# Optimization experiments

Hardware: AMD Instinct MI355X
Metric: run time of the kernel (lower is better)

## Reference

```python
import jax, jax.numpy as jnp
import numpy as np

N = 100000      # nodes
E = 1250000     # edges
F_IN = 32       # node_feat_dim
H = 64          # hidden_dim (hard-coded in module)
R = 8           # num_relations
G = 256         # graphs in batch
EMB = 16        # embedding_dim
OUT = 1         # output_dim
EPS = 1e-5


def setup_inputs() -> dict:
    key = jax.random.key(0)
    ks = jax.random.split(key, 40)
    w = lambda k, shape: (jax.random.normal(k, shape, jnp.float32) * 0.05)
    inp = {
        'x': jax.random.normal(ks[0], (N, F_IN), jnp.float32),
        'edge_index': jax.random.randint(ks[1], (2, E), 0, N),
        'edge_type': jax.random.randint(ks[2], (E,), 0, R),
        'batch': jnp.sort(jax.random.randint(ks[3], (N,), 0, G)),
        # RGCN layer params: per-relation weight, root weight, bias
        'conv1_w': w(ks[4], (R, F_IN, H)), 'conv1_root': w(ks[5], (F_IN, H)), 'conv1_b': jnp.zeros((H,), jnp.float32),
        'bn1_g': jnp.ones((H,), jnp.float32), 'bn1_b': jnp.zeros((H,), jnp.float32),
        'conv2_w': w(ks[6], (R, H, H)), 'conv2_root': w(ks[7], (H, H)), 'conv2_b': jnp.zeros((H,), jnp.float32),
        'bn2_g': jnp.ones((H,), jnp.float32), 'bn2_b': jnp.zeros((H,), jnp.float32),
        'conv3_w': w(ks[8], (R, H, H)), 'conv3_root': w(ks[9], (H, H)), 'conv3_b': jnp.zeros((H,), jnp.float32),
        'bn3_g': jnp.ones((H,), jnp.float32), 'bn3_b': jnp.zeros((H,), jnp.float32),
        # fc_emb: Linear(384->128), BN(128), LeakyReLU, Dropout(eval=id), Linear(128->EMB)
        'fc1_w': w(ks[10], (3 * H * 2, 128)), 'fc1_b': jnp.zeros((128,), jnp.float32),
        'fcbn_g': jnp.ones((128,), jnp.float32), 'fcbn_b': jnp.zeros((128,), jnp.float32),
        'fc2_w': w(ks[11], (128, EMB)), 'fc2_b': jnp.zeros((EMB,), jnp.float32),
        # decoder: Linear(EMB->64), LeakyReLU, Linear(64->OUT)
        'dec1_w': w(ks[12], (EMB, 64)), 'dec1_b': jnp.zeros((64,), jnp.float32),
        'dec2_w': w(ks[13], (64, OUT)), 'dec2_b': jnp.zeros((OUT,), jnp.float32),
    }
    return inp


def _leaky(z):
    return jnp.where(z > 0, z, 0.2 * z)


def _bn(x, g, b):  # training-mode batch norm, biased variance
    mu = x.mean(axis=0)
    var = x.var(axis=0)
    return g * (x - mu) * jax.lax.rsqrt(var + EPS) + b


def _rgcn(x, W, root, bias, src, dst, edge_type):
    # out_i = x_i @ root + bias + sum_r mean_{j in N_r(i)} x_j @ W_r
    out = x @ root + bias
    for r in range(R):
        mask = (edge_type == r).astype(x.dtype)           # [E]
        h = x @ W[r]                                      # [N, out]
        msg = h[src] * mask[:, None]                      # gather + mask
        s = jax.ops.segment_sum(msg, dst, num_segments=N)  # scatter-add
        cnt = jax.ops.segment_sum(mask, dst, num_segments=N)
        out = out + s / jnp.maximum(cnt, 1.0)[:, None]
    return out


def reference(x, edge_index, edge_type, batch,
              conv1_w, conv1_root, conv1_b, bn1_g, bn1_b,
              conv2_w, conv2_root, conv2_b, bn2_g, bn2_b,
              conv3_w, conv3_root, conv3_b, bn3_g, bn3_b,
              fc1_w, fc1_b, fcbn_g, fcbn_b, fc2_w, fc2_b,
              dec1_w, dec1_b, dec2_w, dec2_b):
    src, dst = edge_index[0], edge_index[1]
    x1 = jax.nn.relu(_bn(_rgcn(x, conv1_w, conv1_root, conv1_b, src, dst, edge_type), bn1_g, bn1_b))
    x2 = jax.nn.relu(_bn(_rgcn(x1, conv2_w, conv2_root, conv2_b, src, dst, edge_type), bn2_g, bn2_b))
    x3 = jax.nn.relu(_bn(_rgcn(x2, conv3_w, conv3_root, conv3_b, src, dst, edge_type), bn3_g, bn3_b))
    x_all = jnp.concatenate([x1, x2, x3], axis=1)         # [N, 3H]
    ones = jnp.ones((N,), x.dtype)
    cnt = jax.ops.segment_sum(ones, batch, num_segments=G)
    pool_mean = jax.ops.segment_sum(x_all, batch, num_segments=G) / jnp.maximum(cnt, 1.0)[:, None]
    pool_max = jax.ops.segment_max(x_all, batch, num_segments=G)
    pool_max = jnp.where(jnp.isfinite(pool_max), pool_max, 0.0)
    x_graph = jnp.concatenate([pool_mean, pool_max], axis=1)  # [G, 6H]
    h = _leaky(_bn(x_graph @ fc1_w + fc1_b, fcbn_g, fcbn_b))  # dropout = identity (eval)
    emb = h @ fc2_w + fc2_b                                   # [G, EMB]
    pred = _leaky(emb @ dec1_w + dec1_b) @ dec2_w + dec2_b    # [G, OUT]
    return (pred, emb)
```

## Files before the change

kernel.cpp:

```cpp
#include <hip/hip_runtime.h>

#define NN 100000
#define NE 1250000
#define FIN 32
#define HD 64
#define NR 8
#define NG 256
#define BN_EPS 1e-5f
#define PCH 100
#define M_KEYS (NN * NR)
#define NB 782
#define RREP 32
#define HW 576

#if defined(__has_builtin)
#if __has_builtin(__builtin_amdgcn_fdot2_f32_bf16)
#define USE_DOT2 1
#endif
#endif
#ifndef USE_DOT2
#define USE_DOT2 0
#endif

typedef unsigned short ushort_t;
typedef __attribute__((ext_vector_type(8))) short short8;
typedef __attribute__((ext_vector_type(4))) float f32x4;
typedef __attribute__((ext_vector_type(4))) unsigned int u32x4;
#if USE_DOT2
typedef __bf16 bf16x2 __attribute__((ext_vector_type(2)));
#endif

static __device__ __forceinline__ ushort_t f2bf(float f) {
  unsigned u = __float_as_uint(f);
  u += 0x7fffu + ((u >> 16) & 1u);
  return (ushort_t)(u >> 16);
}
static __device__ __forceinline__ float bf2f(ushort_t b) {
  return __uint_as_float((unsigned)b << 16);
}

__global__ void k_zero(float* __restrict__ p, int n) {
  int i = blockIdx.x * 256 + threadIdx.x;
  if (i < n) p[i] = 0.0f;
}

__global__ void k_cnt(const int* __restrict__ dst, const int* __restrict__ ty,
                      unsigned* __restrict__ cnt, int* __restrict__ rank) {
  int e = blockIdx.x * 256 + threadIdx.x;
  if (e < NE) {
    int key = dst[e] * NR + ty[e];
    rank[e] = (int)atomicAdd(&cnt[key], 1u);
  }
}

__global__ void k_scanA(const unsigned* __restrict__ cnt, unsigned* __restrict__ bsum) {
  __shared__ unsigned red[256];
  int t = threadIdx.x;
  int base = blockIdx.x * 1024 + t * 4;
  unsigned s = 0;
  #pragma unroll
  for (int i = 0; i < 4; i++) {
    int idx = base + i;
    if (idx < M_KEYS) s += cnt[idx];
  }
  red[t] = s;
  __syncthreads();
  for (int off = 128; off > 0; off >>= 1) {
    if (t < off) red[t] += red[t + off];
    __syncthreads();
  }
  if (t == 0) bsum[blockIdx.x] = red[0];
}

__global__ __launch_bounds__(1024) void k_scanB(const unsigned* __restrict__ bsum,
                                                unsigned* __restrict__ boff,
                                                int* __restrict__ rowstart) {
  __shared__ unsigned sb[1024];
  int t = threadIdx.x;
  unsigned mine = (t < NB) ? bsum[t] : 0u;
  sb[t] = mine;
  __syncthreads();
  for (int off = 1; off < 1024; off <<= 1) {
    unsigned v = (t >= off) ? sb[t - off] : 0u;
    __syncthreads();
    sb[t] += v;
    __syncthreads();
  }
  if (t < NB) boff[t] = sb[t] - mine;
  if (t == 1023) rowstart[M_KEYS] = (int)sb[1023];
}

__global__ void k_scanC(const unsigned* __restrict__ cnt, const unsigned* __restrict__ boff,
                        int* __restrict__ rowstart) {
  __shared__ unsigned sb[256];
  int t = threadIdx.x;
  int base = blockIdx.x * 1024 + t * 4;
  unsigned c0 = (base + 0 < M_KEYS) ? cnt[base + 0] : 0u;
  unsigned c1 = (base + 1 < M_KEYS) ? cnt[base + 1] : 0u;
  unsigned c2 = (base + 2 < M_KEYS) ? cnt[base + 2] : 0u;
  unsigned c3 = (base + 3 < M_KEYS) ? cnt[base + 3] : 0u;
  unsigned tot = c0 + c1 + c2 + c3;
  sb[t] = tot;
  __syncthreads();
  for (int off = 1; off < 256; off <<= 1) {
    unsigned v = (t >= off) ? sb[t - off] : 0u;
    __syncthreads();
    sb[t] += v;
    __syncthreads();
  }
  unsigned run = boff[blockIdx.x] + (sb[t] - tot);
  if (base + 0 < M_KEYS) rowstart[base + 0] = (int)run; run += c0;
  if (base + 1 < M_KEYS) rowstart[base + 1] = (int)run; run += c1;
  if (base + 2 < M_KEYS) rowstart[base + 2] = (int)run; run += c2;
  if (base + 3 < M_KEYS) rowstart[base + 3] = (int)run;
}

__global__ void k_place(const int* __restrict__ src, const int* __restrict__ dst,
                        const int* __restrict__ ty, const int* __restrict__ rank,
                        const int* __restrict__ rowstart, unsigned* __restrict__ eb) {
  int e = blockIdx.x * 256 + threadIdx.x;
  if (e < NE) {
    int t = ty[e];
    int key = dst[e] * NR + t;
    unsigned off = (unsigned)(src[e] * HW + t * 64);
    eb[rowstart[key] + rank[e]] = (off << 3) | (unsigned)t;
  }
}

template <int F>
__global__ void k_wconv(const float* __restrict__ convw, const float* __restrict__ root,
                        ushort_t* __restrict__ wt) {
  int i = blockIdx.x * 256 + threadIdx.x;
  if (i >= 576 * F) return;
  int c = i / F, k = i % F;
  float v = (c < 512) ? convw[((size_t)(c >> 6) * F + k) * 64 + (c & 63)]
                      : root[(size_t)k * 64 + (c & 63)];
  wt[(size_t)c * F + k] = f2bf(v);
}

template <int F, bool APPLY_BN>
__global__ __launch_bounds__(256) void k_xmm(
    const float* __restrict__ xin, const float* __restrict__ scsh,
    const ushort_t* __restrict__ wt, ushort_t* __restrict__ h) {
  constexpr int KK = 2 * F;
  constexpr int XPAD = KK + 8;
  constexpr int LDR = 592;
  __shared__ ushort_t xs[16 * XPAD];
  __shared__ ushort_t ot[16 * LDR];
  int lane = threadIdx.x & 63;
  int w = threadIdx.x >> 6;
  int m = lane & 15;
  int q = lane >> 4;
  int ct0 = w * 9;

  short8 bfrag[9 * (F / 32)];
  #pragma unroll
  for (int ks = 0; ks < F / 32; ks++)
    #pragma unroll
    for (int t = 0; t < 9; t++)
      bfrag[ks * 9 + t] =
          *(const short8*)(wt + (size_t)((ct0 + t) * 16 + m) * F + ks * 32 + q * 8);

  for (int tile = blockIdx.x; tile < NN / 16; tile += gridDim.x) {
    int nbase = tile * 16;
    for (int i = threadIdx.x; i < 16 * F; i += 256) {
      int r = i / F, k = i - r * F;
      float v = xin[(size_t)(nbase + r) * F + k];
      if (APPLY_BN) v = fmaxf(fmaf(v, scsh[k], scsh[64 + k]), 0.0f);
      ushort_t hi = f2bf(v);
      xs[r * XPAD + k] = hi;
      xs[r * XPAD + F + k] = f2bf(v - bf2f(hi));
    }
    __syncthreads();

    short8 afrag[2 * (F / 32)];
    #pragma unroll
    for (int ks = 0; ks < F / 32; ks++) {
      afrag[2 * ks + 0] = *(const short8*)&xs[m * XPAD + ks * 32 + q * 8];
      afrag[2 * ks + 1] = *(const short8*)&xs[m * XPAD + F + ks * 32 + q * 8];
    }

    f32x4 acc[9];
    #pragma unroll
    for (int t = 0; t < 9; t++) acc[t] = (f32x4){0.f, 0.f, 0.f, 0.f};
    #pragma unroll
    for (int ks = 0; ks < F / 32; ks++) {
      #pragma unroll
      for (int t = 0; t < 9; t++) {
        acc[t] = __builtin_amdgcn_mfma_f32_16x16x32_bf16(afrag[2 * ks + 0],
                                                         bfrag[ks * 9 + t], acc[t], 0, 0, 0);
        acc[t] = __builtin_amdgcn_mfma_f32_16x16x32_bf16(afrag[2 * ks + 1],
                                                         bfrag[ks * 9 + t], acc[t], 0, 0, 0);
      }
    }
    #pragma unroll
    for (int t = 0; t < 9; t++) {
      int col = (ct0 + t) * 16 + m;
      #pragma unroll
      for (int j = 0; j < 4; j++) {
        int row = q * 4 + j;
        ot[row * LDR + col] = f2bf(acc[t][j]);
      }
    }
    __syncthreads();
    u32x4* dst = (u32x4*)(h + (size_t)nbase * HW);
    for (int idx = threadIdx.x; idx < 16 * 72; idx += 256) {
      int row = idx / 72, i = idx - row * 72;
      dst[row * 72 + i] = *(const u32x4*)&ot[row * LDR + i * 8];
    }
  }
}

__global__ __launch_bounds__(256) void k_agg4(
    const ushort_t* __restrict__ h, const int* __restrict__ rs,
    const unsigned* __restrict__ eb, const float* __restrict__ bias,
    float* __restrict__ outp, float* __restrict__ statsrep) {
  __shared__ float red[1024];
  __shared__ ushort_t iclu[8][8];
  int lane = threadIdx.x & 63, w = threadIdx.x >> 6;
  int hw = lane >> 5;
  int nd = w * 2 + hw;
  int n = blockIdx.x * 8 + nd;
  int l32 = lane & 31;
  if (l32 < 8) {
    int c = rs[n * NR + l32 + 1] - rs[n * NR + l32];
    iclu[nd][l32] = f2bf(1.0f / (float)(c > 1 ? c : 1));
  }
  int lo = rs[n * NR];
  int cnt = rs[n * NR + NR] - lo;
  __syncthreads();
  int g = (lane >> 3) & 3;
  int c8 = (lane & 7) * 8;
  int cntmax = max(cnt, __shfl_xor(cnt, 32));
  float a[8];
  #pragma unroll
  for (int j = 0; j < 8; j++) a[j] = 0.f;
  for (int base = 0; base < cntmax; base += 16) {
    unsigned rec[4]; u32x4 hv[4]; unsigned icb[4];
    #pragma unroll
    for (int s = 0; s < 4; s++) {
      int el = base + s * 4 + g;
      int ee = (el < cnt) ? el : (cnt > 0 ? cnt - 1 : 0);
      rec[s] = eb[lo + ee];
      icb[s] = (el < cnt) ? (unsigned)iclu[nd][rec[s] & 7] : 0u;
    }
    #pragma unroll
    for (int s = 0; s < 4; s++)
      hv[s] = *(const u32x4*)(h + (size_t)(rec[s] >> 3) + c8);
#if USE_DOT2
    #pragma unroll
    for (int s = 0; s < 4; s += 2) {
      unsigned b01 = __builtin_amdgcn_perm(icb[s + 1], icb[s], 0x05040100u);
      bf16x2 bb = __builtin_bit_cast(bf16x2, b01);
      #pragma unroll
      for (int k = 0; k < 4; k++) {
        unsigned plo = __builtin_amdgcn_perm(hv[s + 1][k], hv[s][k], 0x05040100u);
        unsigned phi = __builtin_amdgcn_perm(hv[s + 1][k], hv[s][k], 0x07060302u);
        a[2 * k + 0] = __builtin_amdgcn_fdot2_f32_bf16(
            __builtin_bit_cast(bf16x2, plo), bb, a[2 * k + 0], false);
        a[2 * k + 1] = __builtin_amdgcn_fdot2_f32_bf16(
            __builtin_bit_cast(bf16x2, phi), bb, a[2 * k + 1], false);
      }
    }
#else
    #pragma unroll
    for (int s = 0; s < 4; s++) {
      float ic = bf2f((ushort_t)icb[s]);
      #pragma unroll
      for (int k = 0; k < 4; k++) {
        a[2 * k + 0] = fmaf(__uint_as_float(hv[s][k] << 16), ic, a[2 * k + 0]);
        a[2 * k + 1] = fmaf(__uint_as_float(hv[s][k] & 0xffff0000u), ic, a[2 * k + 1]);
      }
    }
#endif
  }
  #pragma unroll
  for (int j = 0; j < 8; j++) {
    a[j] += __shfl_xor(a[j], 8);
    a[j] += __shfl_xor(a[j], 16);
  }
  if (g == 0) {
    u32x4 sv = *(const u32x4*)(h + (size_t)n * HW + 512 + c8);
    float4 b4lo = *(const float4*)(bias + c8);
    float4 b4hi = *(const float4*)(bias + c8 + 4);
    float d[8];
    d[0] = a[0] + __uint_as_float(sv[0] << 16) + b4lo.x;
    d[1] = a[1] + __uint_as_float(sv[0] & 0xffff0000u) + b4lo.y;
    d[2] = a[2] + __uint_as_float(sv[1] << 16) + b4lo.z;
    d[3] = a[3] + __uint_as_float(sv[1] & 0xffff0000u) + b4lo.w;
    d[4] = a[4] + __uint_as_float(sv[2] << 16) + b4hi.x;
    d[5] = a[5] + __uint_as_float(sv[2] & 0xffff0000u) + b4hi.y;
    d[6] = a[6] + __uint_as_float(sv[3] << 16) + b4hi.z;
    d[7] = a[7] + __uint_as_float(sv[3] & 0xffff0000u) + b4hi.w;
    float4 lo4 = make_float4(d[0], d[1], d[2], d[3]);
    float4 hi4 = make_float4(d[4], d[5], d[6], d[7]);
    *(float4*)(outp + (size_t)n * HD + c8) = lo4;
    *(float4*)(outp + (size_t)n * HD + c8 + 4) = hi4;
    *(float4*)(&red[nd * 64 + c8]) = lo4;
    *(float4*)(&red[nd * 64 + c8 + 4]) = hi4;
    *(float4*)(&red[512 + nd * 64 + c8]) =
        make_float4(d[0] * d[0], d[1] * d[1], d[2] * d[2], d[3] * d[3]);
    *(float4*)(&red[512 + nd * 64 + c8 + 4]) =
        make_float4(d[4] * d[4], d[5] * d[5], d[6] * d[6], d[7] * d[7]);
  }
  __syncthreads();
  if (w == 0) {
    float ts = 0.f, tss = 0.f;
    #pragma unroll
    for (int k = 0; k < 8; k++) {
      ts += red[k * 64 + lane];
      tss += red[512 + k * 64 + lane];
    }
    int rp = blockIdx.x & (RREP - 1);
    atomicAdd(&statsrep[rp * 128 + lane], ts);
    atomicAdd(&statsrep[rp * 128 + 64 + lane], tss);
  }
}

__global__ void k_finstats(const float* __restrict__ rep, const float* __restrict__ g,
                           const float* __restrict__ b, float* __restrict__ scsh) {
  int lane = threadIdx.x;
  float s = 0.f, ss = 0.f;
  for (int rp = 0; rp < RREP; rp++) {
    s += rep[rp * 128 + lane];
    ss += rep[rp * 128 + 64 + lane];
  }
  float mu = s * (1.0f / NN);
  float var = ss * (1.0f / NN) - mu * mu;
  float sc = g[lane] * rsqrtf(var + BN_EPS);
  scsh[lane] = sc;
  scsh[64 + lane] = b[lane] - mu * sc;
}

__global__ void k_poolseg(const float* __restrict__ t1, const float* __restrict__ t2,
                          const float* __restrict__ t3, const float* __restrict__ scsh,
                          const int* __restrict__ batch, float* __restrict__ psum,
                          unsigned* __restrict__ pmax, float* __restrict__ cntg) {
  __shared__ int bsh[PCH];
  int base = blockIdx.x * PCH;
  int c = threadIdx.x;
  for (int i = c; i < PCH; i += 192) bsh[i] = batch[base + i];
  __syncthreads();
  int L = c >> 6, cc = c & 63;
  const float* xs = (L == 0) ? t1 : (L == 1) ? t2 : t3;
  float sc = scsh[L * 128 + cc], sh = scsh[L * 128 + 64 + cc];
  int cur = bsh[0];
  float sum = 0.0f, mx = 0.0f;
  int runlen = 0;
  #pragma unroll 4
  for (int i = 0; i < PCH; i++) {
    int g = bsh[i];
    float v = fmaxf(fmaf(xs[(size_t)(base + i) * 64 + cc], sc, sh), 0.0f);
    if (g != cur) {
      atomicAdd(&psum[cur * 192 + c], sum);
      atomicMax(&pmax[cur * 192 + c], __float_as_uint(mx));
      if (c == 0) atomicAdd(&cntg[cur], (float)runlen);
      cur = g; sum = 0.0f; mx = 0.0f; runlen = 0;
    }
    sum += v;
    mx = fmaxf(mx, v);
    runlen++;
  }
  atomicAdd(&psum[cur * 192 + c], sum);
  atomicMax(&pmax[cur * 192 + c], __float_as_uint(mx));
  if (c == 0) atomicAdd(&cntg[cur], (float)runlen);
}

__global__ void k_fc1(const float* __restrict__ psum, const unsigned* __restrict__ pmax,
                      const float* __restrict__ cntg, const float* __restrict__ w,
                      const float* __restrict__ bias, float* __restrict__ h1) {
  __shared__ float a[384];
  int g = blockIdx.x;
  float ic = 1.0f / fmaxf(cntg[g], 1.0f);
  for (int c = threadIdx.x; c < 384; c += 128) {
    a[c] = (c < 192) ? psum[g * 192 + c] * ic : __uint_as_float(pmax[g * 192 + (c - 192)]);
  }
  __syncthreads();
  int j = threadIdx.x;
  float acc = bias[j];
  for (int k = 0; k < 384; k++) acc = fmaf(a[k], w[k * 128 + j], acc);
  h1[g * 128 + j] = acc;
}

__global__ void k_fcbn_stats(const float* __restrict__ h1, const float* __restrict__ g,
                             const float* __restrict__ b, float* __restrict__ scsh) {
  __shared__ float sr[512], ssr[512];
  int j = threadIdx.x & 127, q = threadIdx.x >> 7;
  float s = 0.f, ss = 0.f;
  for (int i = q * 64; i < q * 64 + 64; i++) {
    float v = h1[i * 128 + j];
    s += v;
    ss = fmaf(v, v, ss);
  }
  sr[threadIdx.x] = s;
  ssr[threadIdx.x] = ss;
  __syncthreads();
  if (q == 0) {
    s = sr[j] + sr[128 + j] + sr[256 + j] + sr[384 + j];
    ss = ssr[j] + ssr[128 + j] + ssr[256 + j] + ssr[384 + j];
    float mu = s * (1.0f / NG);
    float var = ss * (1.0f / NG) - mu * mu;
    float sc = g[j] * rsqrtf(var + BN_EPS);
    scsh[j] = sc;
    scsh[128 + j] = b[j] - mu * sc;
  }
}

__global__ void k_leaky(float* __restrict__ h1, const float* __restrict__ scsh) {
  int j = threadIdx.x;
  int g = blockIdx.x;
  float v = fmaf(h1[g * 128 + j], scsh[j], scsh[128 + j]);
  h1[g * 128 + j] = v > 0.0f ? v : 0.2f * v;
}

__global__ void k_head(const float* __restrict__ h1, const float* __restrict__ fc2w,
                       const float* __restrict__ fc2b, const float* __restrict__ d1w,
                       const float* __restrict__ d1b, const float* __restrict__ d2w,
                       const float* __restrict__ d2b, float* __restrict__ out) {
  __shared__ float emb[16];
  int g = blockIdx.x;
  int t = threadIdx.x;
  if (t < 16) {
    float acc = fc2b[t];
    for (int k = 0; k < 128; k++) acc = fmaf(h1[g * 128 + k], fc2w[k * 16 + t], acc);
    emb[t] = acc;
    out[NG + g * 16 + t] = acc;
  }
  __syncthreads();
  float acc = d1b[t];
  for (int k = 0; k < 16; k++) acc = fmaf(emb[k], d1w[k * 64 + t], acc);
  acc = acc > 0.0f ? acc : 0.2f * acc;
  float p = acc * d2w[t];
  for (int off = 32; off > 0; off >>= 1) p += __shfl_down(p, off);
  if (t == 0) out[g] = p + d2b[0];
}

extern "C" void kernel_launch(void* const* d_in, const int* in_sizes, int n_in,
                              void* d_out, int out_size, void* d_ws, size_t ws_size,
                              hipStream_t stream) {
  const float* x    = (const float*)d_in[0];
  const int*   ei   = (const int*)d_in[1];
  const int*   ety  = (const int*)d_in[2];
  const int*   batch= (const int*)d_in[3];
  const float* c1w  = (const float*)d_in[4];
  const float* c1r  = (const float*)d_in[5];
  const float* c1b  = (const float*)d_in[6];
  const float* bn1g = (const float*)d_in[7];
  const float* bn1b = (const float*)d_in[8];
  const float* c2w  = (const float*)d_in[9];
  const float* c2r  = (const float*)d_in[10];
  const float* c2b  = (const float*)d_in[11];
  const float* bn2g = (const float*)d_in[12];
  const float* bn2b = (const float*)d_in[13];
  const float* c3w  = (const float*)d_in[14];
  const float* c3r  = (const float*)d_in[15];
  const float* c3b  = (const float*)d_in[16];
  const float* bn3g = (const float*)d_in[17];
  const float* bn3b = (const float*)d_in[18];
  const float* fc1w = (const float*)d_in[19];
  const float* fc1b = (const float*)d_in[20];
  const float* fbg  = (const float*)d_in[21];
  const float* fbb  = (const float*)d_in[22];
  const float* fc2w = (const float*)d_in[23];
  const float* fc2b = (const float*)d_in[24];
  const float* d1w  = (const float*)d_in[25];
  const float* d1b  = (const float*)d_in[26];
  const float* d2w  = (const float*)d_in[27];
  const float* d2b  = (const float*)d_in[28];
  const int* esrc = ei;
  const int* edst = ei + NE;
  float* out = (float*)d_out;

  float* W = (float*)d_ws;
  size_t o = 0;
  auto alloc = [&](size_t n) { float* p = W + o; o += (n + 63) & ~(size_t)63; return p; };
  unsigned* cnt      = (unsigned*)alloc(M_KEYS);
  float*    psum     = alloc(NG * 192);
  unsigned* pmax     = (unsigned*)alloc(NG * 192);
  float*    cntg     = alloc(NG);
  float*    statsrep = alloc(3 * RREP * 128);
  size_t zone = o;
  int*      rowstart = (int*)alloc(M_KEYS + 1);
  int*      rank = (int*)alloc(NE);
  unsigned* eb   = (unsigned*)alloc(NE);
  unsigned* bsum = (unsigned*)alloc(1024);
  unsigned* boff = (unsigned*)alloc(1024);
  float*    scsh = alloc(3 * 128);
  float*    fcsc = alloc(256);
  float*    h1   = alloc(NG * 128);
  float*    tmp1 = alloc((size_t)NN * HD);
  float*    tmp2 = alloc((size_t)NN * HD);
  float*    tmp3 = alloc((size_t)NN * HD);
  ushort_t* hbig = (ushort_t*)alloc((size_t)NN * HW / 2);
  ushort_t* wt1  = (ushort_t*)alloc(576 * FIN / 2);
  ushort_t* wt2  = (ushort_t*)alloc(576 * HD / 2);
  ushort_t* wt3  = (ushort_t*)alloc(576 * HD / 2);
  (void)ws_size; (void)in_sizes; (void)n_in; (void)out_size;

  k_zero<<<(int)((zone + 255) / 256), 256, 0, stream>>>(W, (int)zone);
  k_cnt<<<(NE + 255) / 256, 256, 0, stream>>>(edst, ety, cnt, rank);
  k_scanA<<<NB, 256, 0, stream>>>(cnt, bsum);
  k_scanB<<<1, 1024, 0, stream>>>(bsum, boff, rowstart);
  k_scanC<<<NB, 256, 0, stream>>>(cnt, boff, rowstart);
  k_place<<<(NE + 255) / 256, 256, 0, stream>>>(esrc, edst, ety, rank, rowstart, eb);
  k_wconv<FIN><<<(576 * FIN + 255) / 256, 256, 0, stream>>>(c1w, c1r, wt1);
  k_wconv<HD><<<(576 * HD + 255) / 256, 256, 0, stream>>>(c2w, c2r, wt2);
  k_wconv<HD><<<(576 * HD + 255) / 256, 256, 0, stream>>>(c3w, c3r, wt3);

  k_xmm<FIN, false><<<2048, 256, 0, stream>>>(x, nullptr, wt1, hbig);
  k_agg4<<<NN / 8, 256, 0, stream>>>(hbig, rowstart, eb, c1b, tmp1, statsrep);
  k_finstats<<<1, 64, 0, stream>>>(statsrep, bn1g, bn1b, scsh);

  k_xmm<HD, true><<<2048, 256, 0, stream>>>(tmp1, scsh, wt2, hbig);
  k_agg4<<<NN / 8, 256, 0, stream>>>(hbig, rowstart, eb, c2b, tmp2, statsrep + RREP * 128);
  k_finstats<<<1, 64, 0, stream>>>(statsrep + RREP * 128, bn2g, bn2b, scsh + 128);

  k_xmm<HD, true><<<2048, 256, 0, stream>>>(tmp2, scsh + 128, wt3, hbig);
  k_agg4<<<NN / 8, 256, 0, stream>>>(hbig, rowstart, eb, c3b, tmp3, statsrep + 2 * RREP * 128);
  k_finstats<<<1, 64, 0, stream>>>(statsrep + 2 * RREP * 128, bn3g, bn3b, scsh + 256);

  k_poolseg<<<NN / PCH, 192, 0, stream>>>(tmp1, tmp2, tmp3, scsh, batch, psum, pmax, cntg);
  k_fc1<<<NG, 128, 0, stream>>>(psum, pmax, cntg, fc1w, fc1b, h1);
  k_fcbn_stats<<<1, 512, 0, stream>>>(h1, fbg, fbb, fcsc);
  k_leaky<<<NG, 128, 0, stream>>>(h1, fcsc);
  k_head<<<NG, 64, 0, stream>>>(h1, fc2w, fc2b, d1w, d1b, d2w, d2b, out);
}
```

Baseline: 409.4 us.

## Fuse edge counting with first-layer transform into one heterogeneous kernel

Replaces the separate edge-count (atomic rank) kernel and the layer-1 feature transform kernel with a single launch. Odd blocks run the atomic per-(dst,type) counting while even blocks run the MFMA bf16-split x@W transform, so the two independent workloads overlap on the GPU. Weight conversions are moved earlier so wt1 is ready. This saves a launch and lets memory-bound atomics overlap compute, but each half now gets only half the grid.

```diff
diff --git a/kernel.cpp b/kernel.cpp
--- a/kernel.cpp
+++ b/kernel.cpp
@@ -12,6 +12,7 @@
 #define NB 782
 #define RREP 32
 #define HW 576
+#define XCGRID 1792
 
 #if defined(__has_builtin)
 #if __has_builtin(__builtin_amdgcn_fdot2_f32_bf16)
@@ -44,12 +45,82 @@
   if (i < n) p[i] = 0.0f;
 }
 
-__global__ void k_cnt(const int* __restrict__ dst, const int* __restrict__ ty,
-                      unsigned* __restrict__ cnt, int* __restrict__ rank) {
-  int e = blockIdx.x * 256 + threadIdx.x;
-  if (e < NE) {
-    int key = dst[e] * NR + ty[e];
-    rank[e] = (int)atomicAdd(&cnt[key], 1u);
+__global__ __launch_bounds__(256) void k_xc(
+    const float* __restrict__ xin, const ushort_t* __restrict__ wt,
+    ushort_t* __restrict__ h, const int* __restrict__ dst,
+    const int* __restrict__ ty, unsigned* __restrict__ cnt,
+    int* __restrict__ rank) {
+  constexpr int F = FIN;
+  constexpr int KK = 2 * F;
+  constexpr int XPAD = KK + 8;
+  constexpr int LDR = 592;
+  __shared__ ushort_t xs[16 * XPAD];
+  __shared__ ushort_t ot[16 * LDR];
+  if (blockIdx.x & 1) {
+    int stride = (XCGRID / 2) * 256;
+    for (int e = (blockIdx.x >> 1) * 256 + threadIdx.x; e < NE; e += stride) {
+      int key = dst[e] * NR + ty[e];
+      rank[e] = (int)atomicAdd(&cnt[key], 1u);
+    }
+    return;
+  }
+  int lane = threadIdx.x & 63;
+  int w = threadIdx.x >> 6;
+  int m = lane & 15;
+  int q = lane >> 4;
+  int ct0 = w * 9;
+  short8 bfrag[9 * (F / 32)];
+  #pragma unroll
+  for (int ks = 0; ks < F / 32; ks++)
+    #pragma unroll
+    for (int t = 0; t < 9; t++)
+      bfrag[ks * 9 + t] =
+          *(const short8*)(wt + (size_t)((ct0 + t) * 16 + m) * F + ks * 32 + q * 8);
+
+  for (int tile = blockIdx.x >> 1; tile < NN / 16; tile += XCGRID / 2) {
+    int nbase = tile * 16;
+    for (int i = threadIdx.x; i < 16 * F; i += 256) {
+      int r = i / F, k = i - r * F;
+      float v = xin[(size_t)(nbase + r) * F + k];
+      ushort_t hi = f2bf(v);
+      xs[r * XPAD + k] = hi;
+      xs[r * XPAD + F + k] = f2bf(v - bf2f(hi));
+    }
+    __syncthreads();
+    short8 afrag[2 * (F / 32)];
+    #pragma unroll
+    for (int ks = 0; ks < F / 32; ks++) {
+      afrag[2 * ks + 0] = *(const short8*)&xs[m * XPAD + ks * 32 + q * 8];
+      afrag[2 * ks + 1] = *(const short8*)&xs[m * XPAD + F + ks * 32 + q * 8];
+    }
+    f32x4 acc[9];
+    #pragma unroll
+    for (int t = 0; t < 9; t++) acc[t] = (f32x4){0.f, 0.f, 0.f, 0.f};
+    #pragma unroll
+    for (int ks = 0; ks < F / 32; ks++) {
+      #pragma unroll
+      for (int t = 0; t < 9; t++) {
+        acc[t] = __builtin_amdgcn_mfma_f32_16x16x32_bf16(afrag[2 * ks + 0],
+                                                         bfrag[ks * 9 + t], acc[t], 0, 0, 0);
+        acc[t] = __builtin_amdgcn_mfma_f32_16x16x32_bf16(afrag[2 * ks + 1],
+                                                         bfrag[ks * 9 + t], acc[t], 0, 0, 0);
+      }
+    }
+    #pragma unroll
+    for (int t = 0; t < 9; t++) {
+      int col = (ct0 + t) * 16 + m;
+      #pragma unroll
+      for (int j = 0; j < 4; j++) {
+        int row = q * 4 + j;
+        ot[row * LDR + col] = f2bf(acc[t][j]);
+      }
+    }
+    __syncthreads();
+    u32x4* dp = (u32x4*)(h + (size_t)nbase * HW);
+    for (int idx = threadIdx.x; idx < 16 * 72; idx += 256) {
+      int row = idx / 72, i = idx - row * 72;
+      dp[row * 72 + i] = *(const u32x4*)&ot[row * LDR + i * 8];
+    }
   }
 }
 
@@ -498,16 +569,15 @@
   (void)ws_size; (void)in_sizes; (void)n_in; (void)out_size;
 
   k_zero<<<(int)((zone + 255) / 256), 256, 0, stream>>>(W, (int)zone);
-  k_cnt<<<(NE + 255) / 256, 256, 0, stream>>>(edst, ety, cnt, rank);
+  k_wconv<FIN><<<(576 * FIN + 255) / 256, 256, 0, stream>>>(c1w, c1r, wt1);
+  k_wconv<HD><<<(576 * HD + 255) / 256, 256, 0, stream>>>(c2w, c2r, wt2);
+  k_wconv<HD><<<(576 * HD + 255) / 256, 256, 0, stream>>>(c3w, c3r, wt3);
+  k_xc<<<XCGRID, 256, 0, stream>>>(x, wt1, hbig, edst, ety, cnt, rank);
   k_scanA<<<NB, 256, 0, stream>>>(cnt, bsum);
   k_scanB<<<1, 1024, 0, stream>>>(bsum, boff, rowstart);
   k_scanC<<<NB, 256, 0, stream>>>(cnt, boff, rowstart);
   k_place<<<(NE + 255) / 256, 256, 0, stream>>>(esrc, edst, ety, rank, rowstart, eb);
-  k_wconv<FIN><<<(576 * FIN + 255) / 256, 256, 0, stream>>>(c1w, c1r, wt1);
-  k_wconv<HD><<<(576 * HD + 255) / 256, 256, 0, stream>>>(c2w, c2r, wt2);
-  k_wconv<HD><<<(576 * HD + 255) / 256, 256, 0, stream>>>(c3w, c3r, wt3);
-
-  k_xmm<FIN, false><<<2048, 256, 0, stream>>>(x, nullptr, wt1, hbig);
+
   k_agg4<<<NN / 8, 256, 0, stream>>>(hbig, rowstart, eb, c1b, tmp1, statsrep);
   k_finstats<<<1, 64, 0, stream>>>(statsrep, bn1g, bn1b, scsh);
 
```

After: 406.3 us. Within noise of the previous version (-0.8%).
